# Kernel optimization log

Hardware: AMD Instinct MI355X
Metric: run time of the kernel (lower is better)

The kernel has to match this reference:

```python
import jax, jax.numpy as jnp
import numpy as np

B, L, N, F = 8, 12, 1024, 3
H, ND, T, P, NL, GD = 32, 10, 10, 3, 2, 2
ALPHA, PROP = 3.0, 0.05
DOUT = (P + NL - 1) * H  # 128, forced by out_fc_in concat arithmetic


def setup_inputs() -> dict:
    key = jax.random.key(0)
    ks = iter(jax.random.split(key, 48))
    def g(shape, s=0.1):
        return jax.random.normal(next(ks), shape, jnp.float32) * s
    feats = jax.random.normal(next(ks), (B, L, N, F), jnp.float32)
    tid = jax.random.uniform(next(ks), (B, L, N, 1), jnp.float32, 0.0, 1.0 - 1e-4)
    diw = jax.random.randint(next(ks), (B, L, N, 1), 0, 7).astype(jnp.float32)
    history_data = jnp.concatenate([feats, tid, diw], axis=-1)
    return {
        'history_data': history_data,
        'W_emb': g((F, H)), 'b_emb': g((H,)),
        'T_emb': g((288, T)), 'D_emb': g((7, T)),
        'node_u': g((N, ND)), 'node_d': g((N, ND)),
        'W_std': g((P - 1, H + ND + 2 * T, H)), 'b_std': g((P - 1, H)),
        'W_mlp': g((P + 1, H, 1)), 'b_mlp': g((P + 1, 1)),
        'W_start': g((32, L)), 'b_start': g((32,)),
        'W_g': g((NL, H, H)),
        'W_rnn': g((H, DOUT)), 'b_rnn': g((DOUT,)),
        'W_e1': g((128, 32)), 'b_e1': g((128,)),
        'W_e2': g((L, 128)), 'b_e2': g((L,)),
        'M': g((N, DOUT), 1.0),
        'W_f1': g((2 * P * H + NL * H + 2 * T, 512)), 'b_f1': g((512,)),
        'W_f2': g((512, 3)), 'b_f2': g((3,)),
        'W_e3': g((4, L)), 'b_e3': g((4,)),
    }


def reference(history_data, W_emb, b_emb, T_emb, D_emb, node_u, node_d,
              W_std, b_std, W_mlp, b_mlp, W_start, b_start, W_g,
              W_rnn, b_rnn, W_e1, b_e1, W_e2, b_e2, M,
              W_f1, b_f1, W_f2, b_f2, W_e3, b_e3):
    feats = history_data[..., :F]
    tid_idx = (history_data[..., F] * 288).astype(jnp.int32)   # [B,L,N]
    diw_idx = history_data[..., F + 1].astype(jnp.int32)
    tid = T_emb[tid_idx]  # [B,L,N,T] gather
    diw = D_emb[diw_idx]
    hist = feats @ W_emb + b_emb  # [B,L,N,H] embedding

    # STD decomposition: gated filters peel off P-1 pattern components
    node_b = jnp.broadcast_to(node_u[None, None], (B, L, N, ND))
    xs, resid = [], hist
    for i in range(P - 1):
        inp = jnp.concatenate([hist, node_b, tid, diw], axis=-1)
        xi = jax.nn.sigmoid(inp @ W_std[i] + b_std[i]) * hist
        xs.append(xi)
        resid = resid - xi
    xs.append(resid)

    # Node_Clusterer (vectorized argmin routing + batch-mode)
    hist_mean = jnp.mean(hist @ W_mlp[0] + b_mlp[0], axis=1)  # [B,N,1]
    x_mean = jnp.concatenate(
        [jnp.mean(xs[p] @ W_mlp[p + 1] + b_mlp[p + 1], axis=1) for p in range(P)],
        axis=-1)  # [B,N,P]
    ratio = x_mean / (hist_mean + 1e-6)
    centers = jnp.max(ratio, axis=1, keepdims=True)  # [B,1,P]
    dist = jnp.abs(ratio - centers)
    assign = jnp.argmin(dist, axis=-1)  # [B,N]
    counts = jnp.sum(jax.nn.one_hot(assign, P, dtype=jnp.float32), axis=0)  # [N,P]
    label = jnp.argmax(counts, axis=-1)  # [N] mode over batch (ties -> smallest)
    masks = jax.nn.one_hot(label, P, dtype=jnp.float32).T  # [P,N]
    h0 = jnp.concatenate(xs, axis=-1)  # [B,L,N,P*H]

    # DSTGNN: learned directed adjacency
    m1, m2 = jnp.tanh(ALPHA * node_u), jnp.tanh(ALPHA * node_d)
    A = jax.nn.relu(jnp.tanh(ALPHA * (m1 @ m2.T - m2 @ m1.T)))  # [N,N]

    # SIE: per-pattern masked residual GCN on the clustered subgraphs
    x0 = jnp.einsum('cl,blnh->bcnh', W_start, hist) + b_start[None, :, None, None]
    out = jnp.zeros((B, 32, N, H), jnp.float32)
    for p in range(P):
        mp = masks[p]
        Ap = A * mp[:, None] * mp[None, :]
        Ap = Ap / (jnp.sum(Ap, axis=1, keepdims=True) + 1e-6)
        acc = jnp.zeros_like(x0)
        for l in range(NL):
            h = x0
            for _ in range(GD):
                h = PROP * x0 + (1.0 - PROP) * jnp.einsum('nm,bcmh->bcnh', Ap, h)
            acc = acc + jnp.einsum('bcnh,hk->bcnk', h, W_g[l])
        out = out + acc * mp[None, None, :, None]

    x_out = jnp.tanh(out @ W_rnn + b_rnn)  # [B,32,N,128]
    x_out = jax.nn.relu(jnp.einsum('oc,bcnh->bonh', W_e1, x_out) + b_e1[None, :, None, None])
    x_out = jnp.einsum('oc,bcnh->bonh', W_e2, x_out) + b_e2[None, :, None, None]  # [B,12,N,128]
    x_out = x_out * M[None, None]  # LearnableMatrixModel per-node scale

    fh = jnp.concatenate([x_out, hist, h0, tid, diw], axis=-1)  # [B,12,N,276]
    fc = jax.nn.relu(jax.nn.relu(fh) @ W_f1 + b_f1) @ W_f2 + b_f2  # [B,12,N,3]
    fc = jnp.einsum('oc,bcnh->bonh', W_e3, fc) + b_e3[None, :, None, None]  # [B,4,N,3]
    return jnp.transpose(fc, (0, 2, 1, 3)).reshape(B, N, -1)  # [B,N,12]
```

## Files before the change

### kernel.cpp

```cpp
#include <hip/hip_runtime.h>
#include <math.h>

#define BB 8
#define LL 12
#define NN 1024
#define FF 3
#define HH 32
#define NDD 10
#define TTT 10
#define PP 3
#define DOUTT 128
constexpr float kALPHA = 3.0f;

typedef __attribute__((ext_vector_type(8))) short short8v;
typedef __attribute__((ext_vector_type(4))) float float4v;

__device__ __forceinline__ unsigned short f2bf(float x) {
    union { float f; unsigned u; } v; v.f = x;
    unsigned r = v.u + 0x7FFF + ((v.u >> 16) & 1);
    return (unsigned short)(r >> 16);
}
__device__ __forceinline__ float bf2f(unsigned short u) {
    union { unsigned u; float f; } v; v.u = ((unsigned)u) << 16;
    return v.f;
}

__device__ __forceinline__ void gload_lds16(const unsigned short* g, unsigned short* l) {
    __builtin_amdgcn_global_load_lds(
        (const __attribute__((address_space(1))) void*)g,
        (__attribute__((address_space(3))) void*)l,
        16, 0, 0);
}

__device__ __forceinline__ void stage_tile(const unsigned short* __restrict__ g, int stride,
                                           unsigned short* tile, int tid) {
#pragma unroll
    for (int rr = 0; rr < 2; rr++) {
        int c = rr*256 + tid;
        int row = c >> 2;
        int q = (c & 3) ^ ((row >> 1) & 3);
        gload_lds16(g + (size_t)row*stride + q*8,
                    tile + ((size_t)(rr*256 + (tid & 192)))*8);
    }
}

__device__ __forceinline__ void stage_tileA512(const unsigned short* __restrict__ g, int stride,
                                               unsigned short* tile, int tid) {
    int row = tid >> 2;
    int q = (tid & 3) ^ ((row >> 1) & 3);
    gload_lds16(g + (size_t)row*stride + q*8,
                tile + ((size_t)(tid & ~63))*8);
}

__device__ __forceinline__ void stage_tileB512(const unsigned short* __restrict__ g, int stride,
                                               unsigned short* tile, int tid) {
#pragma unroll
    for (int rr = 0; rr < 4; rr++) {
        int c = rr*512 + tid;
        int row = c >> 2;
        int q = (c & 3) ^ ((row >> 1) & 3);
        gload_lds16(g + (size_t)row*stride + q*8,
                    tile + ((size_t)(rr*512 + (tid & ~63)))*8);
    }
}

constexpr size_t OFF_HIST    = 0;
constexpr size_t OFF_S4      = OFF_HIST   + (size_t)BB*LL*NN*HH;
constexpr size_t OFF_RATIO   = OFF_S4     + (size_t)BB*LL*NN*4;
constexpr size_t OFF_CENT    = OFF_RATIO  + (size_t)BB*NN*3;
constexpr size_t OFF_M1      = OFF_CENT   + 32;
constexpr size_t OFF_M2      = OFF_M1     + (size_t)NN*NDD;
constexpr size_t OFF_LABEL   = OFF_M2     + (size_t)NN*NDD;
constexpr size_t OFF_AN      = OFF_LABEL  + NN;
constexpr size_t OFF_ACOMBB  = OFF_AN     + (size_t)NN*NN;
constexpr size_t OFF_X0      = OFF_ACOMBB + (size_t)NN*NN/2;
constexpr size_t OFF_HFINB   = OFF_X0     + (size_t)NN*BB*HH*HH;
constexpr size_t OFF_WCOMBOT = OFF_HFINB  + (size_t)NN*BB*HH*HH/2;
constexpr size_t OFF_WE1B    = OFF_WCOMBOT+ 1024*4;
constexpr size_t OFF_FC      = OFF_WE1B   + 1024*4;
constexpr size_t OFF_ANB     = OFF_FC     + (size_t)BB*LL*NN*3;
constexpr size_t OFF_ANBT    = OFF_ANB    + (size_t)NN*NN/2;
constexpr size_t OFF_X0T     = OFF_ANBT   + (size_t)NN*NN/2;
constexpr size_t OFF_W1HI    = OFF_X0T    + (size_t)BB*HH*HH*NN/2;
constexpr size_t OFF_FHB     = OFF_W1HI   + (size_t)512*288/2;
constexpr size_t WS_FLOATS   = OFF_FHB    + (size_t)BB*LL*NN*288/2;

__global__ __launch_bounds__(256) void k1_embed(
    const float* __restrict__ hd, const float* __restrict__ W_emb, const float* __restrict__ b_emb,
    const float* __restrict__ T_emb, const float* __restrict__ D_emb, const float* __restrict__ node_u,
    const float* __restrict__ W_std, const float* __restrict__ b_std,
    const float* __restrict__ W_mlp, const float* __restrict__ b_mlp,
    float* __restrict__ hist, unsigned short* __restrict__ fhB, float* __restrict__ s4)
{
    __shared__ float sW[2*62*32];
    for (int i = threadIdx.x; i < 2*62*32; i += 256) sW[i] = W_std[i];
    __syncthreads();

    int pos = blockIdx.x*256 + threadIdx.x;
    int n = pos & (NN-1);
    const float* hp = hd + (size_t)pos*5;
    float f0 = hp[0], f1 = hp[1], f2 = hp[2];
    int ti = (int)(hp[3]*288.0f);
    int di = (int)hp[4];

    float tv[10], dv[10], nu[10];
#pragma unroll
    for (int t = 0; t < 10; t++) {
        tv[t] = T_emb[ti*10+t]; dv[t] = D_emb[di*10+t]; nu[t] = node_u[n*10+t];
    }
    float h[32];
#pragma unroll
    for (int j = 0; j < 32; j++) h[j] = b_emb[j] + f0*W_emb[j] + f1*W_emb[32+j] + f2*W_emb[64+j];

    float a0[32], a1[32];
#pragma unroll
    for (int j = 0; j < 32; j++) { a0[j] = b_std[j]; a1[j] = b_std[32+j]; }

    auto accum = [&](float v, int i) {
#pragma unroll
        for (int q = 0; q < 8; q++) {
            float4 w0 = *(const float4*)&sW[i*32 + q*4];
            float4 w1 = *(const float4*)&sW[(62+i)*32 + q*4];
            a0[q*4+0] += v*w0.x; a0[q*4+1] += v*w0.y; a0[q*4+2] += v*w0.z; a0[q*4+3] += v*w0.w;
            a1[q*4+0] += v*w1.x; a1[q*4+1] += v*w1.y; a1[q*4+2] += v*w1.z; a1[q*4+3] += v*w1.w;
        }
    };
#pragma unroll
    for (int i = 0; i < 32; i++) accum(h[i], i);
#pragma unroll
    for (int i = 0; i < 10; i++) accum(nu[i], 32+i);
#pragma unroll
    for (int i = 0; i < 10; i++) accum(tv[i], 42+i);
#pragma unroll
    for (int i = 0; i < 10; i++) accum(dv[i], 52+i);

    float x0v[32], x1v[32], rv[32];
    float s0 = b_mlp[0], s1 = b_mlp[1], s2 = b_mlp[2], s3 = b_mlp[3];
#pragma unroll
    for (int j = 0; j < 32; j++) {
        float sg0 = 1.f/(1.f + __expf(-a0[j]));
        float sg1 = 1.f/(1.f + __expf(-a1[j]));
        x0v[j] = sg0*h[j]; x1v[j] = sg1*h[j]; rv[j] = h[j] - x0v[j] - x1v[j];
        s0 += h[j]  * W_mlp[j];
        s1 += x0v[j]* W_mlp[32+j];
        s2 += x1v[j]* W_mlp[64+j];
        s3 += rv[j] * W_mlp[96+j];
    }
    float* ho = hist + (size_t)pos*32;
#pragma unroll
    for (int q = 0; q < 8; q++)
        *(float4*)&ho[q*4] = make_float4(h[q*4], h[q*4+1], h[q*4+2], h[q*4+3]);

    unsigned short* fr = fhB + (size_t)pos*288;
#pragma unroll
    for (int q = 0; q < 4; q++) {
        short8v v;
#pragma unroll
        for (int e = 0; e < 8; e++) v[e] = (short)f2bf(fmaxf(h[q*8+e], 0.f));
        *(short8v*)&fr[128 + q*8] = v;
    }
#pragma unroll
    for (int q = 0; q < 4; q++) {
        short8v v;
#pragma unroll
        for (int e = 0; e < 8; e++) v[e] = (short)f2bf(fmaxf(x0v[q*8+e], 0.f));
        *(short8v*)&fr[160 + q*8] = v;
    }
#pragma unroll
    for (int q = 0; q < 4; q++) {
        short8v v;
#pragma unroll
        for (int e = 0; e < 8; e++) v[e] = (short)f2bf(fmaxf(x1v[q*8+e], 0.f));
        *(short8v*)&fr[192 + q*8] = v;
    }
#pragma unroll
    for (int q = 0; q < 4; q++) {
        short8v v;
#pragma unroll
        for (int e = 0; e < 8; e++) v[e] = (short)f2bf(fmaxf(rv[q*8+e], 0.f));
        *(short8v*)&fr[224 + q*8] = v;
    }
    float tail[32];
#pragma unroll
    for (int i = 0; i < 32; i++) tail[i] = (i < 10) ? tv[i] : ((i < 20) ? dv[i-10] : 0.f);
#pragma unroll
    for (int q = 0; q < 4; q++) {
        short8v v;
#pragma unroll
        for (int e = 0; e < 8; e++) v[e] = (short)f2bf(fmaxf(tail[q*8+e], 0.f));
        *(short8v*)&fr[256 + q*8] = v;
    }
    *(float4*)&s4[(size_t)pos*4] = make_float4(s0, s1, s2, s3);
}

__global__ void k2_ratio(const float* __restrict__ s4, float* __restrict__ ratio)
{
    int bn = blockIdx.x*256 + threadIdx.x;
    if (bn >= BB*NN) return;
    int b = bn >> 10, n = bn & 1023;
    float a0=0, a1=0, a2=0, a3=0;
    for (int l = 0; l < 12; l++) {
        const float* sp = s4 + ((size_t)(b*12+l)*NN + n)*4;
        a0 += sp[0]; a1 += sp[1]; a2 += sp[2]; a3 += sp[3];
    }
    float hm = a0/12.f;
    float* rp = ratio + (size_t)bn*3;
    rp[0] = (a1/12.f)/(hm + 1e-6f);
    rp[1] = (a2/12.f)/(hm + 1e-6f);
    rp[2] = (a3/12.f)/(hm + 1e-6f);
}

__global__ __launch_bounds__(256) void k3_centers(const float* __restrict__ ratio, float* __restrict__ centers)
{
    int b = blockIdx.x;
    float m0=-3.4e38f, m1v=-3.4e38f, m2v=-3.4e38f;
    for (int n = threadIdx.x; n < NN; n += 256) {
        const float* rp = ratio + ((size_t)b*NN + n)*3;
        m0 = fmaxf(m0, rp[0]); m1v = fmaxf(m1v, rp[1]); m2v = fmaxf(m2v, rp[2]);
    }
#pragma unroll
    for (int off = 32; off > 0; off >>= 1) {
        m0  = fmaxf(m0,  __shfl_down(m0,  off));
        m1v = fmaxf(m1v, __shfl_down(m1v, off));
        m2v = fmaxf(m2v, __shfl_down(m2v, off));
    }
    __shared__ float red[4][3];
    int wid = threadIdx.x >> 6, lane = threadIdx.x & 63;
    if (lane == 0) { red[wid][0]=m0; red[wid][1]=m1v; red[wid][2]=m2v; }
    __syncthreads();
    if (threadIdx.x == 0) {
        centers[b*3+0] = fmaxf(fmaxf(red[0][0],red[1][0]), fmaxf(red[2][0],red[3][0]));
        centers[b*3+1] = fmaxf(fmaxf(red[0][1],red[1][1]), fmaxf(red[2][1],red[3][1]));
        centers[b*3+2] = fmaxf(fmaxf(red[0][2],red[1][2]), fmaxf(red[2][2],red[3][2]));
    }
}

__global__ void k4_labels(const float* __restrict__ ratio, const float* __restrict__ centers,
                          const float* __restrict__ node_u, const float* __restrict__ node_d,
                          int* __restrict__ label, float* __restrict__ m1, float* __restrict__ m2)
{
    int n = blockIdx.x*256 + threadIdx.x;
    if (n >= NN) return;
    int c0=0, c1=0, c2=0;
    for (int b = 0; b < BB; b++) {
        const float* rp = ratio + ((size_t)b*NN + n)*3;
        const float* cp = centers + b*3;
        float d0 = fabsf(rp[0]-cp[0]), d1 = fabsf(rp[1]-cp[1]), d2 = fabsf(rp[2]-cp[2]);
        int a = 0; float best = d0;
        if (d1 < best) { best = d1; a = 1; }
        if (d2 < best) { best = d2; a = 2; }
        if (a == 0) c0++; else if (a == 1) c1++; else c2++;
    }
    int lab = 0, bc = c0;
    if (c1 > bc) { bc = c1; lab = 1; }
    if (c2 > bc) { bc = c2; lab = 2; }
    label[n] = lab;
#pragma unroll
    for (int d = 0; d < 10; d++) {
        m1[n*10+d] = tanhf(kALPHA*node_u[n*10+d]);
        m2[n*10+d] = tanhf(kALPHA*node_d[n*10+d]);
    }
}

__global__ __launch_bounds__(256) void k5_A(const float* __restrict__ m1, const float* __restrict__ m2,
                                            const int* __restrict__ label, float* __restrict__ An)
{
    int n = blockIdx.x;
    __shared__ float row[1024];
    __shared__ float m1n[10], m2n[10];
    __shared__ float ssum[4];
    int t = threadIdx.x;
    if (t < 10) { m1n[t] = m1[n*10+t]; m2n[t] = m2[n*10+t]; }
    __syncthreads();
    int labn = label[n];
    float lsum = 0.f;
    for (int m = t; m < 1024; m += 256) {
        float a = 0.f;
        if (label[m] == labn) {
            float x = 0.f;
#pragma unroll
            for (int d = 0; d < 10; d++) x += m1n[d]*m2[m*10+d] - m2n[d]*m1[m*10+d];
            a = fmaxf(tanhf(3.f*x), 0.f);
        }
        row[m] = a; lsum += a;
    }
#pragma unroll
    for (int off = 32; off > 0; off >>= 1) lsum += __shfl_down(lsum, off);
    int wid = t >> 6, lane = t & 63;
    if (lane == 0) ssum[wid] = lsum;
    __syncthreads();
    float inv = 1.f/((ssum[0]+ssum[1]+ssum[2]+ssum[3]) + 1e-6f);
    for (int m = t; m < 1024; m += 256) An[(size_t)n*1024 + m] = row[m]*inv;
}

template<bool ALSO_DIRECT>
__global__ __launch_bounds__(256) void kt_transpose(const float* __restrict__ in,
                                                    unsigned short* __restrict__ outT,
                                                    unsigned short* __restrict__ outD,
                                                    int R, int C)
{
    __shared__ float tile[64][65];
    int c0 = blockIdx.x*64, r0 = blockIdx.y*64;
    for (int i = threadIdx.x; i < 64*64; i += 256) {
        int r = i >> 6, c = i & 63;
        float v = in[(size_t)(r0+r)*C + c0+c];
        tile[r][c] = v;
        if (ALSO_DIRECT) outD[(size_t)(r0+r)*C + c0+c] = f2bf(v);
    }
    __syncthreads();
    for (int i = threadIdx.x; i < 64*64; i += 256) {
        int c = i >> 6, r = i & 63;
        outT[(size_t)(c0+c)*R + r0+r] = f2bf(tile[r][c]);
    }
}

template<int MODE>
__global__ __launch_bounds__(256) void gemm_mfma(
    const unsigned short* __restrict__ A, const unsigned short* __restrict__ B,
    void* __restrict__ Cout, int Nout, int K)
{
    __shared__ __align__(16) unsigned short lds[2][2][2][128*32];
    const int t = threadIdx.x;

    int id = blockIdx.x + gridDim.x*blockIdx.y;
    int gx8 = gridDim.x >> 3;
    int xcd = id & 7, local = id >> 3;
    int bx = xcd*gx8 + (local % gx8);
    int by = local / gx8;

    const int lane = t & 63, wid = t >> 6;
    const int wr = wid >> 1, wc = wid & 1;
    const int l15 = lane & 15, l4 = lane >> 4;
    const int swq8 = (l4 ^ ((l15 >> 1) & 3))*8;
    const int row0 = by*128, col0 = bx*128;

    float4v acc[4][4];
#pragma unroll
    for (int i = 0; i < 4; i++)
#pragma unroll
        for (int j = 0; j < 4; j++) acc[i][j] = (float4v){0.f,0.f,0.f,0.f};

    const unsigned short* Ab = A + (size_t)row0*K;
    const unsigned short* Bb = B + (size_t)col0*K;

    stage_tile(Ab +  0, K, lds[0][0][0], t); stage_tile(Bb +  0, K, lds[0][1][0], t);
    stage_tile(Ab + 32, K, lds[0][0][1], t); stage_tile(Bb + 32, K, lds[0][1][1], t);
    __syncthreads();

    const int nk = K >> 6;
    for (int ks = 0; ks < nk; ks++) {
        int cur = ks & 1;
        if (ks + 1 < nk) {
            stage_tile(Ab + (ks+1)*64,      K, lds[cur^1][0][0], t);
            stage_tile(Bb + (ks+1)*64,      K, lds[cur^1][1][0], t);
            stage_tile(Ab + (ks+1)*64 + 32, K, lds[cur^1][0][1], t);
            stage_tile(Bb + (ks+1)*64 + 32, K, lds[cur^1][1][1], t);
        }
#pragma unroll
        for (int kk = 0; kk < 2; kk++) {
            short8v a[4], b[4];
#pragma unroll
            for (int f = 0; f < 4; f++) {
                a[f] = *(const short8v*)&lds[cur][0][kk][(wr*64 + f*16 + l15)*32 + swq8];
                b[f] = *(const short8v*)&lds[cur][1][kk][(wc*64 + f*16 + l15)*32 + swq8];
            }
#pragma unroll
            for (int i = 0; i < 4; i++)
#pragma unroll
                for (int j = 0; j < 4; j++)
                    acc[i][j] = __builtin_amdgcn_mfma_f32_16x16x32_bf16(a[i], b[j], acc[i][j], 0, 0, 0);
        }
        __syncthreads();
    }

#pragma unroll
    for (int i = 0; i < 4; i++) {
#pragma unroll
        for (int j = 0; j < 4; j++) {
            int gc = col0 + wc*64 + j*16 + l15;
#pragma unroll
            for (int r = 0; r < 4; r++) {
                int gr = row0 + wr*64 + i*16 + l4*4 + r;
                if (MODE == 0) {
                    float an = bf2f(A[(size_t)gr*K + gc]);
                    float v = 0.9025f*acc[i][j][r] + 0.0475f*an + ((gr==gc) ? 0.05f : 0.f);
                    ((unsigned short*)Cout)[(size_t)gr*Nout + gc] = f2bf(v);
                } else {
                    ((unsigned short*)Cout)[(size_t)gr*Nout + gc] = f2bf(acc[i][j][r]);
                }
            }
        }
    }
}

__global__ __launch_bounds__(256) void k7t_x0T(
    const float* __restrict__ hist, const float* __restrict__ W_start, const float* __restrict__ b_start,
    unsigned short* __restrict__ x0T)
{
    __shared__ float hl[12*1056];
    __shared__ float sw[384];
    __shared__ float sb[32];

    const int b = blockIdx.x >> 5;
    const int n0 = (blockIdx.x & 31)*32;
    const int t = threadIdx.x;

    for (int i = t; i < 384; i += 256) sw[i] = W_start[i];
    if (t < 32) sb[t] = b_start[t];
#pragma unroll
    for (int l = 0; l < 12; l++) {
        float4 v = ((const float4*)(hist + ((size_t)(b*12+l)*NN + n0)*32))[t];
        int nn = t >> 3, h4 = (t & 7)*4;
        float* d = &hl[l*1056 + nn*33 + h4];
        d[0] = v.x; d[1] = v.y; d[2] = v.z; d[3] = v.w;
    }
    __syncthreads();

    const int n = t & 31;
    const int c0base = t >> 5;
    for (int it = 0; it < 128; it++) {
        int col = c0base + it*8;
        int c = col >> 5, h = col & 31;
        float s = sb[c];
#pragma unroll
        for (int l = 0; l < 12; l++) s += sw[c*12+l]*hl[l*1056 + n*33 + h];
        x0T[((size_t)(b*1024 + col))*1024 + n0 + n] = f2bf(s);
    }
}

__global__ void kw_combo2(const float* __restrict__ W_g, const float* __restrict__ W_rnn,
                          const float* __restrict__ W_e1,
                          unsigned short* __restrict__ wcomboT, unsigned short* __restrict__ we1B)
{
    int j = threadIdx.x;
    for (int hh = 0; hh < 32; hh++) {
        float s = 0.f;
        for (int k = 0; k < 32; k++) s += (W_g[hh*32+k] + W_g[1024 + hh*32+k]) * W_rnn[k*128 + j];
        wcomboT[j*32 + hh] = f2bf(s);
    }
    for (int i = j; i < 4096; i += 128) we1B[i] = f2bf(W_e1[i]);
}

__global__ __launch_bounds__(256) void k9_mfma(
    const unsigned short* __restrict__ hfinB,
    const unsigned short* __restrict__ wcomboT,
    const float* __restrict__ b_rnn,
    const unsigned short* __restrict__ we1B,
    const float* __restrict__ b_e1,
    const float* __restrict__ W_e2,
    const float* __restrict__ b_e2,
    const float* __restrict__ Mm,
    unsigned short* __restrict__ fhB)
{
    __shared__ __align__(16) unsigned short xrT[4][1024];
    __shared__ float sWe2T[128][12];
    __shared__ float sBe1[128];
    __shared__ float sBe2[16];

    const int t = threadIdx.x;
    const int bid = blockIdx.x;
    const int n = bid & (NN-1), b = bid >> 10;
    const int lane = t & 63, wid = t >> 6;
    const int l15 = lane & 15, l4 = lane >> 4;
    const int j0 = wid*32;

    for (int i = t; i < 12*128; i += 256) {
        int o2 = i >> 7, o1 = i & 127;
        sWe2T[o1][o2] = W_e2[i];
    }
    if (t < 128) sBe1[t] = b_e1[t];
    if (t < 12)  sBe2[t] = b_e2[t];
    __syncthreads();

    const unsigned short* Hb = hfinB + (size_t)n*8192 + (size_t)b*1024;
    short8v ah[2], bw[2];
#pragma unroll
    for (int f = 0; f < 2; f++) {
        ah[f] = *(const short8v*)&Hb[(f*16 + l15)*32 + l4*8];
        bw[f] = *(const short8v*)&wcomboT[(j0 + f*16 + l15)*32 + l4*8];
    }
    float br[2];
    br[0] = b_rnn[j0 + l15];
    br[1] = b_rnn[j0 + 16 + l15];
    float4v accA[2][2];
#pragma unroll
    for (int cf = 0; cf < 2; cf++)
#pragma unroll
        for (int jf = 0; jf < 2; jf++)
            accA[cf][jf] = (float4v){br[jf], br[jf], br[jf], br[jf]};
#pragma unroll
    for (int cf = 0; cf < 2; cf++)
#pragma unroll
        for (int jf = 0; jf < 2; jf++)
            accA[cf][jf] = __builtin_amdgcn_mfma_f32_16x16x32_bf16(ah[cf], bw[jf], accA[cf][jf], 0, 0, 0);

#pragma unroll
    for (int cf = 0; cf < 2; cf++)
#pragma unroll
        for (int jf = 0; jf < 2; jf++) {
            int jl = jf*16 + l15;
            int csw = (cf*16 + l4*4) ^ ((jl & 3) << 3);
            unsigned short p0 = f2bf(tanhf(accA[cf][jf][0]));
            unsigned short p1 = f2bf(tanhf(accA[cf][jf][1]));
            unsigned short p2 = f2bf(tanhf(accA[cf][jf][2]));
            unsigned short p3 = f2bf(tanhf(accA[cf][jf][3]));
            unsigned int lo = (unsigned)p0 | ((unsigned)p1 << 16);
            unsigned int hi = (unsigned)p2 | ((unsigned)p3 << 16);
            *(uint2*)&xrT[wid][jl*32 + csw] = make_uint2(lo, hi);
        }

    short8v bx[2];
#pragma unroll
    for (int jf = 0; jf < 2; jf++) {
        int jl = jf*16 + l15;
        int csw = (l4*8) ^ ((jl & 3) << 3);
        bx[jf] = *(const short8v*)&xrT[wid][jl*32 + csw];
    }
    float4v accB[8][2];
#pragma unroll
    for (int of = 0; of < 8; of++)
#pragma unroll
        for (int jf = 0; jf < 2; jf++) accB[of][jf] = (float4v){0.f,0.f,0.f,0.f};
#pragma unroll
    for (int of = 0; of < 8; of++) {
        short8v aw = *(const short8v*)&we1B[(of*16 + l15)*32 + l4*8];
        accB[of][0] = __builtin_amdgcn_mfma_f32_16x16x32_bf16(aw, bx[0], accB[of][0], 0, 0, 0);
        accB[of][1] = __builtin_amdgcn_mfma_f32_16x16x32_bf16(aw, bx[1], accB[of][1], 0, 0, 0);
    }

    float v0[12], v1[12];
#pragma unroll
    for (int o2 = 0; o2 < 12; o2++) { v0[o2] = 0.f; v1[o2] = 0.f; }
#pragma unroll
    for (int of = 0; of < 8; of++) {
#pragma unroll
        for (int r = 0; r < 4; r++) {
            int o1 = of*16 + l4*4 + r;
            float be = sBe1[o1];
            float z0 = fmaxf(accB[of][0][r] + be, 0.f);
            float z1 = fmaxf(accB[of][1][r] + be, 0.f);
#pragma unroll
            for (int q = 0; q < 3; q++) {
                float4 w = *(const float4*)&sWe2T[o1][q*4];
                v0[q*4+0] += w.x*z0; v0[q*4+1] += w.y*z0; v0[q*4+2] += w.z*z0; v0[q*4+3] += w.w*z0;
                v1[q*4+0] += w.x*z1; v1[q*4+1] += w.y*z1; v1[q*4+2] += w.z*z1; v1[q*4+3] += w.w*z1;
            }
        }
    }
#pragma unroll
    for (int o2 = 0; o2 < 12; o2++) {
        v0[o2] += __shfl_xor(v0[o2], 16);
        v0[o2] += __shfl_xor(v0[o2], 32);
        v1[o2] += __shfl_xor(v1[o2], 16);
        v1[o2] += __shfl_xor(v1[o2], 32);
    }

    float mm0 = Mm[(size_t)n*128 + j0 + l15];
    float mm1 = Mm[(size_t)n*128 + j0 + 16 + l15];
#pragma unroll
    for (int e = 0; e < 3; e++) {
        int o2 = l4*3 + e;
        float be2 = sBe2[o2];
        size_t base = ((size_t)((b*12 + o2)*NN + n))*288;
        float val0 = (v0[o2] + be2) * mm0;
        float val1 = (v1[o2] + be2) * mm1;
        fhB[base + j0 + l15]      = f2bf(fmaxf(val0, 0.f));
        fhB[base + j0 + 16 + l15] = f2bf(fmaxf(val1, 0.f));
    }
}

__global__ void kt_w1(const float* __restrict__ W_f1, unsigned short* __restrict__ w1hi)
{
    int idx = blockIdx.x*256 + threadIdx.x;
    if (idx >= 512*288) return;
    int n = idx / 288, k = idx - n*288;
    float w = (k < 276) ? W_f1[(size_t)k*512 + n] : 0.f;
    w1hi[idx] = f2bf(w);
}

__global__ __launch_bounds__(512, 2) void k10_mfma2(
    const unsigned short* __restrict__ fhB, const unsigned short* __restrict__ w1hi,
    const float* __restrict__ b_f1, const float* __restrict__ W_f2, float* __restrict__ fc)
{
    __shared__ __align__(16) unsigned short smem[40960];
    unsigned short (*Abuf)[128*32]  = (unsigned short(*)[128*32])smem;
    unsigned short (*Bhbuf)[512*32] = (unsigned short(*)[512*32])(smem + 8192);
    float* fcp = (float*)smem;

    const int t = threadIdx.x;
    int id = blockIdx.x;
    int by = (id & 7)*96 + (id >> 3);
    const int pos0 = by*128;

    const int lane = t & 63, w = t >> 6;
    const int wr = w >> 2, wc = w & 3;
    const int l15 = lane & 15, l4 = lane >> 4;
    const int swq8 = (l4 ^ ((l15 >> 1) & 3))*8;

    float4v acc[4][8];
#pragma unroll
    for (int i = 0; i < 4; i++)
#pragma unroll
        for (int j = 0; j < 8; j++) acc[i][j] = (float4v){0.f,0.f,0.f,0.f};

    const unsigned short* Ab = fhB + (size_t)pos0*288;

    stage_tileA512(Ab,   288, Abuf[0],  t);
    stage_tileB512(w1hi, 288, Bhbuf[0], t);
    __syncthreads();

    for (int ks = 0; ks < 9; ks++) {
        int cur = ks & 1;
        if (ks + 1 < 9) {
            stage_tileA512(Ab   + (ks+1)*32, 288, Abuf[cur^1],  t);
            stage_tileB512(w1hi + (ks+1)*32, 288, Bhbuf[cur^1], t);
        }
        short8v a[4];
#pragma unroll
        for (int f = 0; f < 4; f++)
            a[f] = *(const short8v*)&Abuf[cur][(wr*64 + f*16 + l15)*32 + swq8];
#pragma unroll
        for (int j = 0; j < 8; j++) {
            int brow = wc*128 + j*16 + l15;
            short8v bh = *(const short8v*)&Bhbuf[cur][brow*32 + swq8];
#pragma unroll
            for (int i = 0; i < 4; i++)
                acc[i][j] = __builtin_amdgcn_mfma_f32_16x16x32_bf16(a[i], bh, acc[i][j], 0, 0, 0);
        }
        __syncthreads();
    }

    for (int i = t; i < 384; i += 512) fcp[i] = 0.f;
    __syncthreads();

    float pk[4][4][3];
#pragma unroll
    for (int i = 0; i < 4; i++)
#pragma unroll
        for (int r = 0; r < 4; r++)
#pragma unroll
            for (int k = 0; k < 3; k++) pk[i][r][k] = 0.f;

#pragma unroll
    for (int j = 0; j < 8; j++) {
        int gc = wc*128 + j*16 + l15;
        float bias = b_f1[gc];
        float w20 = W_f2[gc*3+0], w21 = W_f2[gc*3+1], w22 = W_f2[gc*3+2];
#pragma unroll
        for (int i = 0; i < 4; i++)
#pragma unroll
            for (int r = 0; r < 4; r++) {
                float z = fmaxf(acc[i][j][r] + bias, 0.f);
                pk[i][r][0] += z*w20; pk[i][r][1] += z*w21; pk[i][r][2] += z*w22;
            }
    }
#pragma unroll
    for (int i = 0; i < 4; i++)
#pragma unroll
        for (int r = 0; r < 4; r++) {
            int rowL = wr*64 + i*16 + l4*4 + r;
            atomicAdd(&fcp[rowL*3 + 0], pk[i][r][0]);
            atomicAdd(&fcp[rowL*3 + 1], pk[i][r][1]);
            atomicAdd(&fcp[rowL*3 + 2], pk[i][r][2]);
        }
    __syncthreads();
    for (int i = t; i < 384; i += 512) {
        fc[(size_t)pos0*3 + i] = fcp[i];
    }
}

__global__ void k11_e3(const float* __restrict__ fc, const float* __restrict__ b_f2,
                       const float* __restrict__ W_e3, const float* __restrict__ b_e3,
                       float* __restrict__ out)
{
    int idx = blockIdx.x*256 + threadIdx.x;
    if (idx >= BB*NN*12) return;
    int ok = idx % 12;
    int o = ok / 3, k = ok % 3;
    int bn = idx / 12;
    int n = bn & 1023, b = bn >> 10;
    float s = b_e3[o];
    float bk = b_f2[k];
#pragma unroll
    for (int c = 0; c < 12; c++)
        s += W_e3[o*12+c] * (fc[((size_t)(b*12+c)*NN + n)*3 + k] + bk);
    out[idx] = s;
}

extern "C" void kernel_launch(void* const* d_in, const int* in_sizes, int n_in,
                              void* d_out, int out_size, void* d_ws, size_t ws_size,
                              hipStream_t stream)
{
    const float* hd      = (const float*)d_in[0];
    const float* W_emb   = (const float*)d_in[1];
    const float* b_emb   = (const float*)d_in[2];
    const float* T_emb   = (const float*)d_in[3];
    const float* D_emb   = (const float*)d_in[4];
    const float* node_u  = (const float*)d_in[5];
    const float* node_d  = (const float*)d_in[6];
    const float* W_std   = (const float*)d_in[7];
    const float* b_std   = (const float*)d_in[8];
    const float* W_mlp   = (const float*)d_in[9];
    const float* b_mlp   = (const float*)d_in[10];
    const float* W_start = (const float*)d_in[11];
    const float* b_start = (const float*)d_in[12];
    const float* W_g     = (const float*)d_in[13];
    const float* W_rnn   = (const float*)d_in[14];
    const float* b_rnn   = (const float*)d_in[15];
    const float* W_e1    = (const float*)d_in[16];
    const float* b_e1    = (const float*)d_in[17];
    const float* W_e2    = (const float*)d_in[18];
    const float* b_e2    = (const float*)d_in[19];
    const float* Mm      = (const float*)d_in[20];
    const float* W_f1    = (const float*)d_in[21];
    const float* b_f1    = (const float*)d_in[22];
    const float* W_f2    = (const float*)d_in[23];
    const float* b_f2    = (const float*)d_in[24];
    const float* W_e3    = (const float*)d_in[25];
    const float* b_e3    = (const float*)d_in[26];

    float* ws      = (float*)d_ws;
    float* hist    = ws + OFF_HIST;
    float* s4      = ws + OFF_S4;
    float* ratio   = ws + OFF_RATIO;
    float* cent    = ws + OFF_CENT;
    float* m1      = ws + OFF_M1;
    float* m2      = ws + OFF_M2;
    int*   label   = (int*)(ws + OFF_LABEL);
    float* An      = ws + OFF_AN;
    unsigned short* AcombB  = (unsigned short*)(ws + OFF_ACOMBB);
    unsigned short* hfinB   = (unsigned short*)(ws + OFF_HFINB);
    unsigned short* wcomboT = (unsigned short*)(ws + OFF_WCOMBOT);
    unsigned short* we1B    = (unsigned short*)(ws + OFF_WE1B);
    float* fc      = ws + OFF_FC;
    unsigned short* AnB   = (unsigned short*)(ws + OFF_ANB);
    unsigned short* AnBT  = (unsigned short*)(ws + OFF_ANBT);
    unsigned short* x0T   = (unsigned short*)(ws + OFF_X0T);
    unsigned short* w1hi  = (unsigned short*)(ws + OFF_W1HI);
    unsigned short* fhB   = (unsigned short*)(ws + OFF_FHB);

    k1_embed<<<(BB*LL*NN)/256, 256, 0, stream>>>(hd, W_emb, b_emb, T_emb, D_emb, node_u,
                                                 W_std, b_std, W_mlp, b_mlp, hist, fhB, s4);
    k2_ratio<<<(BB*NN)/256, 256, 0, stream>>>(s4, ratio);
    k3_centers<<<BB, 256, 0, stream>>>(ratio, cent);
    k4_labels<<<NN/256, 256, 0, stream>>>(ratio, cent, node_u, node_d, label, m1, m2);
    k5_A<<<NN, 256, 0, stream>>>(m1, m2, label, An);
    kt_transpose<true><<<dim3(16, 16), 256, 0, stream>>>(An, AnBT, AnB, 1024, 1024);
    gemm_mfma<0><<<dim3(8, 8), 256, 0, stream>>>(AnB, AnBT, AcombB, 1024, 1024);
    k7t_x0T<<<256, 256, 0, stream>>>(hist, W_start, b_start, x0T);
    gemm_mfma<2><<<dim3(64, 8), 256, 0, stream>>>(AcombB, x0T, hfinB, 8192, 1024);
    kw_combo2<<<1, 128, 0, stream>>>(W_g, W_rnn, W_e1, wcomboT, we1B);
    k9_mfma<<<BB*NN, 256, 0, stream>>>(hfinB, wcomboT, b_rnn, we1B, b_e1, W_e2, b_e2, Mm, fhB);
    kt_w1<<<(512*288)/256, 256, 0, stream>>>(W_f1, w1hi);
    k10_mfma2<<<768, 512, 0, stream>>>(fhB, w1hi, b_f1, W_f2, fc);
    k11_e3<<<(BB*NN*12)/256, 256, 0, stream>>>(fc, b_f2, W_e3, b_e3, (float*)d_out);
}
```

Before: 398.1 us.

## Split FC1 GEMM output columns across two blocks with partial-sum buffers

```diff
diff --git a/kernel.cpp b/kernel.cpp
--- a/kernel.cpp
+++ b/kernel.cpp
@@ -52,10 +52,10 @@
                 tile + ((size_t)(tid & ~63))*8);
 }
 
-__device__ __forceinline__ void stage_tileB512(const unsigned short* __restrict__ g, int stride,
-                                               unsigned short* tile, int tid) {
-#pragma unroll
-    for (int rr = 0; rr < 4; rr++) {
+__device__ __forceinline__ void stage_tile256_512(const unsigned short* __restrict__ g, int stride,
+                                                  unsigned short* tile, int tid) {
+#pragma unroll
+    for (int rr = 0; rr < 2; rr++) {
         int c = rr*512 + tid;
         int row = c >> 2;
         int q = (c & 3) ^ ((row >> 1) & 3);
@@ -73,8 +73,8 @@
 constexpr size_t OFF_LABEL   = OFF_M2     + (size_t)NN*NDD;
 constexpr size_t OFF_AN      = OFF_LABEL  + NN;
 constexpr size_t OFF_ACOMBB  = OFF_AN     + (size_t)NN*NN;
-constexpr size_t OFF_X0      = OFF_ACOMBB + (size_t)NN*NN/2;
-constexpr size_t OFF_HFINB   = OFF_X0     + (size_t)NN*BB*HH*HH;
+constexpr size_t OFF_FC1     = OFF_ACOMBB + (size_t)NN*NN/2;
+constexpr size_t OFF_HFINB   = OFF_FC1    + (size_t)NN*BB*HH*HH;
 constexpr size_t OFF_WCOMBOT = OFF_HFINB  + (size_t)NN*BB*HH*HH/2;
 constexpr size_t OFF_WE1B    = OFF_WCOMBOT+ 1024*4;
 constexpr size_t OFF_FC      = OFF_WE1B   + 1024*4;
@@ -578,55 +578,57 @@
     w1hi[idx] = f2bf(w);
 }
 
-__global__ __launch_bounds__(512, 2) void k10_mfma2(
+__global__ __launch_bounds__(512, 2) void k10_mfma3(
     const unsigned short* __restrict__ fhB, const unsigned short* __restrict__ w1hi,
-    const float* __restrict__ b_f1, const float* __restrict__ W_f2, float* __restrict__ fc)
-{
-    __shared__ __align__(16) unsigned short smem[40960];
-    unsigned short (*Abuf)[128*32]  = (unsigned short(*)[128*32])smem;
-    unsigned short (*Bhbuf)[512*32] = (unsigned short(*)[512*32])(smem + 8192);
+    const float* __restrict__ b_f1, const float* __restrict__ W_f2,
+    float* __restrict__ fc0, float* __restrict__ fc1)
+{
+    __shared__ __align__(16) unsigned short smem[24576];
+    unsigned short (*Abuf)[128*32] = (unsigned short(*)[128*32])smem;
+    unsigned short (*Bbuf)[256*32] = (unsigned short(*)[256*32])(smem + 8192);
     float* fcp = (float*)smem;
 
     const int t = threadIdx.x;
     int id = blockIdx.x;
-    int by = (id & 7)*96 + (id >> 3);
-    const int pos0 = by*128;
+    int sid = (id & 7)*192 + (id >> 3);
+    const int by = sid >> 1, bx = sid & 1;
+    const int pos0 = by*128, col0 = bx*256;
 
     const int lane = t & 63, w = t >> 6;
     const int wr = w >> 2, wc = w & 3;
     const int l15 = lane & 15, l4 = lane >> 4;
     const int swq8 = (l4 ^ ((l15 >> 1) & 3))*8;
 
-    float4v acc[4][8];
+    float4v acc[4][4];
 #pragma unroll
     for (int i = 0; i < 4; i++)
 #pragma unroll
-        for (int j = 0; j < 8; j++) acc[i][j] = (float4v){0.f,0.f,0.f,0.f};
-
-    const unsigned short* Ab = fhB + (size_t)pos0*288;
-
-    stage_tileA512(Ab,   288, Abuf[0],  t);
-    stage_tileB512(w1hi, 288, Bhbuf[0], t);
+        for (int j = 0; j < 4; j++) acc[i][j] = (float4v){0.f,0.f,0.f,0.f};
+
+    const unsigned short* Ab = fhB  + (size_t)pos0*288;
+    const unsigned short* Bb = w1hi + (size_t)col0*288;
+
+    stage_tileA512(Ab, 288, Abuf[0], t);
+    stage_tile256_512(Bb, 288, Bbuf[0], t);
     __syncthreads();
 
     for (int ks = 0; ks < 9; ks++) {
         int cur = ks & 1;
         if (ks + 1 < 9) {
-            stage_tileA512(Ab   + (ks+1)*32, 288, Abuf[cur^1],  t);
-            stage_tileB512(w1hi + (ks+1)*32, 288, Bhbuf[cur^1], t);
-        }
-        short8v a[4];
-#pragma unroll
-        for (int f = 0; f < 4; f++)
+            stage_tileA512(Ab + (ks+1)*32, 288, Abuf[cur^1], t);
+            stage_tile256_512(Bb + (ks+1)*32, 288, Bbuf[cur^1], t);
+        }
+        short8v a[4], b[4];
+#pragma unroll
+        for (int f = 0; f < 4; f++) {
             a[f] = *(const short8v*)&Abuf[cur][(wr*64 + f*16 + l15)*32 + swq8];
-#pragma unroll
-        for (int j = 0; j < 8; j++) {
-            int brow = wc*128 + j*16 + l15;
-            short8v bh = *(const short8v*)&Bhbuf[cur][brow*32 + swq8];
-#pragma unroll
-            for (int i = 0; i < 4; i++)
-                acc[i][j] = __builtin_amdgcn_mfma_f32_16x16x32_bf16(a[i], bh, acc[i][j], 0, 0, 0);
-        }
+            b[f] = *(const short8v*)&Bbuf[cur][(wc*64 + f*16 + l15)*32 + swq8];
+        }
+#pragma unroll
+        for (int i = 0; i < 4; i++)
+#pragma unroll
+            for (int j = 0; j < 4; j++)
+                acc[i][j] = __builtin_amdgcn_mfma_f32_16x16x32_bf16(a[i], b[j], acc[i][j], 0, 0, 0);
         __syncthreads();
     }
 
@@ -642,8 +644,8 @@
             for (int k = 0; k < 3; k++) pk[i][r][k] = 0.f;
 
 #pragma unroll
-    for (int j = 0; j < 8; j++) {
-        int gc = wc*128 + j*16 + l15;
+    for (int j = 0; j < 4; j++) {
+        int gc = col0 + wc*64 + j*16 + l15;
         float bias = b_f1[gc];
         float w20 = W_f2[gc*3+0], w21 = W_f2[gc*3+1], w22 = W_f2[gc*3+2];
 #pragma unroll
@@ -664,12 +666,14 @@
             atomicAdd(&fcp[rowL*3 + 2], pk[i][r][2]);
         }
     __syncthreads();
+    float* fcout = bx ? fc1 : fc0;
     for (int i = t; i < 384; i += 512) {
-        fc[(size_t)pos0*3 + i] = fcp[i];
-    }
-}
-
-__global__ void k11_e3(const float* __restrict__ fc, const float* __restrict__ b_f2,
+        fcout[(size_t)pos0*3 + i] = fcp[i];
+    }
+}
+
+__global__ void k11_e3(const float* __restrict__ fc0, const float* __restrict__ fc1,
+                       const float* __restrict__ b_f2,
                        const float* __restrict__ W_e3, const float* __restrict__ b_e3,
                        float* __restrict__ out)
 {
@@ -682,8 +686,10 @@
     float s = b_e3[o];
     float bk = b_f2[k];
 #pragma unroll
-    for (int c = 0; c < 12; c++)
-        s += W_e3[o*12+c] * (fc[((size_t)(b*12+c)*NN + n)*3 + k] + bk);
+    for (int c = 0; c < 12; c++) {
+        size_t p = ((size_t)(b*12+c)*NN + n)*3 + k;
+        s += W_e3[o*12+c] * (fc0[p] + fc1[p] + bk);
+    }
     out[idx] = s;
 }
 
@@ -732,7 +738,8 @@
     unsigned short* hfinB   = (unsigned short*)(ws + OFF_HFINB);
     unsigned short* wcomboT = (unsigned short*)(ws + OFF_WCOMBOT);
     unsigned short* we1B    = (unsigned short*)(ws + OFF_WE1B);
-    float* fc      = ws + OFF_FC;
+    float* fc0     = ws + OFF_FC;
+    float* fc1     = ws + OFF_FC1;
     unsigned short* AnB   = (unsigned short*)(ws + OFF_ANB);
     unsigned short* AnBT  = (unsigned short*)(ws + OFF_ANBT);
     unsigned short* x0T   = (unsigned short*)(ws + OFF_X0T);
@@ -752,6 +759,6 @@
     kw_combo2<<<1, 128, 0, stream>>>(W_g, W_rnn, W_e1, wcomboT, we1B);
     k9_mfma<<<BB*NN, 256, 0, stream>>>(hfinB, wcomboT, b_rnn, we1B, b_e1, W_e2, b_e2, Mm, fhB);
     kt_w1<<<(512*288)/256, 256, 0, stream>>>(W_f1, w1hi);
-    k10_mfma2<<<768, 512, 0, stream>>>(fhB, w1hi, b_f1, W_f2, fc);
-    k11_e3<<<(BB*NN*12)/256, 256, 0, stream>>>(fc, b_f2, W_e3, b_e3, (float*)d_out);
-}
+    k10_mfma3<<<1536, 512, 0, stream>>>(fhB, w1hi, b_f1, W_f2, fc0, fc1);
+    k11_e3<<<(BB*NN*12)/256, 256, 0, stream>>>(fc0, fc1, b_f2, W_e3, b_e3, (float*)d_out);
+}
```

New measurement: 512.8 us. 1.29x slower.

## Replace propagation GEMM with 256x128-tile double-buffered 512-thread kernel

Applied to the files above, without the earlier changes.

```diff
diff --git a/kernel.cpp b/kernel.cpp
--- a/kernel.cpp
+++ b/kernel.cpp
@@ -50,6 +50,18 @@
     int q = (tid & 3) ^ ((row >> 1) & 3);
     gload_lds16(g + (size_t)row*stride + q*8,
                 tile + ((size_t)(tid & ~63))*8);
+}
+
+__device__ __forceinline__ void stage_tile256_512(const unsigned short* __restrict__ g, int stride,
+                                                  unsigned short* tile, int tid) {
+#pragma unroll
+    for (int rr = 0; rr < 2; rr++) {
+        int c = rr*512 + tid;
+        int row = c >> 2;
+        int q = (c & 3) ^ ((row >> 1) & 3);
+        gload_lds16(g + (size_t)row*stride + q*8,
+                    tile + ((size_t)(rr*512 + (tid & ~63)))*8);
+    }
 }
 
 __device__ __forceinline__ void stage_tileB512(const unsigned short* __restrict__ g, int stride,
@@ -388,6 +400,78 @@
                 } else {
                     ((unsigned short*)Cout)[(size_t)gr*Nout + gc] = f2bf(acc[i][j][r]);
                 }
+            }
+        }
+    }
+}
+
+__global__ __launch_bounds__(512, 2) void gemm2_big(
+    const unsigned short* __restrict__ A, const unsigned short* __restrict__ B,
+    unsigned short* __restrict__ Cout)
+{
+    __shared__ __align__(16) unsigned short Abuf[2][2][256*32];
+    __shared__ __align__(16) unsigned short Bbuf[2][2][128*32];
+
+    const int t = threadIdx.x;
+    int id = blockIdx.x;
+    int sid = (id & 7)*32 + (id >> 3);
+    const int by = sid >> 6, bx = sid & 63;
+    const int row0 = by*256, col0 = bx*128;
+
+    const int lane = t & 63, w = t >> 6;
+    const int wr = w >> 1, wc = w & 1;
+    const int l15 = lane & 15, l4 = lane >> 4;
+    const int swq8 = (l4 ^ ((l15 >> 1) & 3))*8;
+
+    float4v acc[4][4];
+#pragma unroll
+    for (int i = 0; i < 4; i++)
+#pragma unroll
+        for (int j = 0; j < 4; j++) acc[i][j] = (float4v){0.f,0.f,0.f,0.f};
+
+    const unsigned short* Ab = A + (size_t)row0*1024;
+    const unsigned short* Bb = B + (size_t)col0*1024;
+
+    stage_tile256_512(Ab +  0, 1024, Abuf[0][0], t);
+    stage_tile256_512(Ab + 32, 1024, Abuf[0][1], t);
+    stage_tileA512(Bb +  0, 1024, Bbuf[0][0], t);
+    stage_tileA512(Bb + 32, 1024, Bbuf[0][1], t);
+    __syncthreads();
+
+    for (int ks = 0; ks < 16; ks++) {
+        int cur = ks & 1;
+        if (ks + 1 < 16) {
+            stage_tile256_512(Ab + (ks+1)*64,      1024, Abuf[cur^1][0], t);
+            stage_tile256_512(Ab + (ks+1)*64 + 32, 1024, Abuf[cur^1][1], t);
+            stage_tileA512(Bb + (ks+1)*64,      1024, Bbuf[cur^1][0], t);
+            stage_tileA512(Bb + (ks+1)*64 + 32, 1024, Bbuf[cur^1][1], t);
+        }
+#pragma unroll
+        for (int kk = 0; kk < 2; kk++) {
+            short8v a[4], b[4];
+#pragma unroll
+            for (int f = 0; f < 4; f++) {
+                a[f] = *(const short8v*)&Abuf[cur][kk][(wr*64 + f*16 + l15)*32 + swq8];
+                b[f] = *(const short8v*)&Bbuf[cur][kk][(wc*64 + f*16 + l15)*32 + swq8];
+            }
+#pragma unroll
+            for (int i = 0; i < 4; i++)
+#pragma unroll
+                for (int j = 0; j < 4; j++)
+                    acc[i][j] = __builtin_amdgcn_mfma_f32_16x16x32_bf16(a[i], b[j], acc[i][j], 0, 0, 0);
+        }
+        __syncthreads();
+    }
+
+#pragma unroll
+    for (int i = 0; i < 4; i++) {
+#pragma unroll
+        for (int j = 0; j < 4; j++) {
+            int gc = col0 + wc*64 + j*16 + l15;
+#pragma unroll
+            for (int r = 0; r < 4; r++) {
+                int gr = row0 + wr*64 + i*16 + l4*4 + r;
+                Cout[(size_t)gr*8192 + gc] = f2bf(acc[i][j][r]);
             }
         }
     }
@@ -748,7 +832,7 @@
     kt_transpose<true><<<dim3(16, 16), 256, 0, stream>>>(An, AnBT, AnB, 1024, 1024);
     gemm_mfma<0><<<dim3(8, 8), 256, 0, stream>>>(AnB, AnBT, AcombB, 1024, 1024);
     k7t_x0T<<<256, 256, 0, stream>>>(hist, W_start, b_start, x0T);
-    gemm_mfma<2><<<dim3(64, 8), 256, 0, stream>>>(AcombB, x0T, hfinB, 8192, 1024);
+    gemm2_big<<<256, 512, 0, stream>>>(AcombB, x0T, hfinB);
     kw_combo2<<<1, 128, 0, stream>>>(W_g, W_rnn, W_e1, wcomboT, we1B);
     k9_mfma<<<BB*NN, 256, 0, stream>>>(hfinB, wcomboT, b_rnn, we1B, b_e1, W_e2, b_e2, Mm, fhB);
     kt_w1<<<(512*288)/256, 256, 0, stream>>>(W_f1, w1hi);
```

Result: slower. 408.3 us (+2.6%).
